# Kernel optimization log

Hardware: AMD Instinct MI355X
Metric: run time of the kernel (lower is better)

Reference implementation:

```python
import jax, jax.numpy as jnp
import numpy as np

N = 50000
E = 800000
F_IN = 128
HEADS = 4
OUT_PER_HEAD = 32  # out_features 128 / 4 heads
NEG_SLOPE = 0.2


def setup_inputs() -> dict:
    key = jax.random.key(0)
    k1, k2, k3, k4, k5 = jax.random.split(key, 5)
    x = jax.random.normal(k1, (N, F_IN), dtype=jnp.float32)
    edge_index = jax.random.randint(k2, (2, E), 0, N, dtype=jnp.int64)
    # xavier-uniform style init
    limW = float(np.sqrt(6.0 / (F_IN + OUT_PER_HEAD)))
    W = jax.random.uniform(k3, (HEADS, F_IN, OUT_PER_HEAD), jnp.float32, -limW, limW)
    lima = float(np.sqrt(6.0 / (OUT_PER_HEAD + 1)))
    a_l = jax.random.uniform(k4, (HEADS, OUT_PER_HEAD), jnp.float32, -lima, lima)
    a_r = jax.random.uniform(k5, (HEADS, OUT_PER_HEAD), jnp.float32, -lima, lima)
    return {"x": x, "edge_index": edge_index, "W": W, "a_l": a_l, "a_r": a_r}


def _leaky_relu(v, slope):
    return jnp.where(v >= 0, v, slope * v)


def reference(x, edge_index, W, a_l, a_r):
    src, dst = edge_index[0], edge_index[1]
    n = x.shape[0]
    # Wh: [heads, N, out_per_head]
    Wh = jnp.einsum('nf,kfh->knh', x, W)
    e_l = jnp.einsum('knh,kh->kn', Wh, a_l)  # [heads, N]
    e_r = jnp.einsum('knh,kh->kn', Wh, a_r)
    # per-edge attention logits [heads, E]
    e = _leaky_relu(e_l[:, src] + e_r[:, dst], NEG_SLOPE)
    # segment softmax over incoming edges of each dst node
    seg_max = jax.vmap(lambda ee: jax.ops.segment_max(ee, dst, num_segments=n))(e)
    seg_max = jnp.maximum(seg_max, -1e9)  # torch init value for empty nodes
    exp_e = jnp.exp(e - seg_max[:, dst])
    denom = jax.vmap(lambda ee: jax.ops.segment_sum(ee, dst, num_segments=n))(exp_e)
    alpha = exp_e / (denom[:, dst] + 1e-16)  # [heads, E]
    # weighted aggregation: [heads, E, out_per_head] scattered into [heads, N, out_per_head]
    weighted = alpha[..., None] * Wh[:, src, :]
    out = jax.vmap(lambda w: jax.ops.segment_sum(w, dst, num_segments=n))(weighted)
    # concat heads -> [N, heads*out_per_head]
    return out.transpose(1, 0, 2).reshape(n, -1)
```

## Files before the change

### kernel.cpp

```cpp
#include <hip/hip_runtime.h>

#define NN 50000
#define NE 800000
#define FIN 128
#define NH 4
#define OPH 32
#define FOUT 128
#define NSLOPE 0.2f
#define NGB ((NN + 63) / 64)
#define BCOLS 144
#define LDA 136
#define BSH 5
#define BUKSZ 32
#define NBUK ((NN + BUKSZ - 1) >> BSH)
#define CHUNK 8192
#define NPB1 ((NE + CHUNK - 1) / CHUNK)
#define SLOTP 32
#define SLOTQ 31
#define SLOTS 64
#define GRID1 (9 * NPB1)

typedef __attribute__((ext_vector_type(8))) short short8v;
typedef __attribute__((ext_vector_type(4))) float f32x4;

static __device__ __forceinline__ unsigned short f2bf(float f) {
  unsigned int u = __float_as_uint(f);
  u += 0x7fffu + ((u >> 16) & 1u);
  return (unsigned short)(u >> 16);
}

__global__ __launch_bounds__(128) void k_prep(
    const float* __restrict__ W, const float* __restrict__ a_l,
    const float* __restrict__ a_r, unsigned short* __restrict__ Bt) {
  const int c = blockIdx.x;
  const int f = threadIdx.x;
  unsigned short v = 0;
  if (c < 128) {
    const int h = c >> 5, o = c & 31;
    v = f2bf(W[h * (FIN * OPH) + f * OPH + o]);
  } else if (c < 136) {
    const int j = c - 128;
    const int h = j & 3;
    const float* __restrict__ av = (j < 4) ? a_l : a_r;
    float s = 0.f;
    for (int o = 0; o < 32; ++o)
      s += W[h * (FIN * OPH) + f * OPH + o] * av[h * OPH + o];
    v = f2bf(s);
  }
  Bt[c * FIN + f] = v;
}

__global__ __launch_bounds__(256) void k_gemm_part(
    const float* __restrict__ x, const unsigned short* __restrict__ Bt,
    const int* __restrict__ src, const int* __restrict__ dst,
    unsigned int* __restrict__ ebuf,
    unsigned short* __restrict__ WhU, float* __restrict__ e_l4,
    float* __restrict__ e_r4) {
  __shared__ union U {
    unsigned short As[64 * LDA];
    int cntl[NBUK];
  } sh;
  const int t = threadIdx.x;
  const int bid = blockIdx.x;

  if ((bid % 9) == 8) {
    const int part = bid / 9;
    const int base = part * CHUNK;
    for (int b = t; b < NBUK; b += 256) sh.cntl[b] = 0;
    __syncthreads();
    unsigned int* __restrict__ myreg = ebuf + (size_t)part * NBUK * SLOTP;
#pragma unroll
    for (int k = 0; k < CHUNK / 256; ++k) {
      const int i = base + k * 256 + t;
      if (i < NE) {
        const int d = dst[i];
        const unsigned int s = (unsigned int)src[i];
        const int b = d >> BSH;
        const int lp = atomicAdd(&sh.cntl[b], 1);
        if (lp < SLOTQ)
          myreg[b * SLOTP + 1 + lp] =
              ((unsigned int)(d & (BUKSZ - 1)) << 16) | s;
      }
    }
    __syncthreads();
    for (int b = t; b < NBUK; b += 256)
      myreg[b * SLOTP] = (unsigned int)min(sh.cntl[b], SLOTQ);
    return;
  }

  const int g = bid - (bid + 1) / 9;
  if (g >= NGB) return;
  const int m0 = g * 64;

#pragma unroll
  for (int i = 0; i < 8; ++i) {
    const int fidx = t + i * 256;
    const int node = fidx >> 5;
    const int fg = fidx & 31;
    const int n = m0 + node;
    float4 v = make_float4(0.f, 0.f, 0.f, 0.f);
    if (n < NN) v = *(const float4*)(x + (size_t)n * FIN + fg * 4);
    ushort4 pk;
    pk.x = f2bf(v.x); pk.y = f2bf(v.y); pk.z = f2bf(v.z); pk.w = f2bf(v.w);
    *(ushort4*)&sh.As[node * LDA + fg * 4] = pk;
  }
  __syncthreads();

  const int w = t >> 6;
  const int l = t & 63;
  const int lr = l & 15;
  const int lk = l >> 4;

  short8v a_frag[4];
#pragma unroll
  for (int kk = 0; kk < 4; ++kk)
    a_frag[kk] = *(const short8v*)&sh.As[(w * 16 + lr) * LDA + kk * 32 + lk * 8];

  f32x4 acc[9];
#pragma unroll
  for (int ct = 0; ct < 9; ++ct) acc[ct] = (f32x4){0.f, 0.f, 0.f, 0.f};

#pragma unroll
  for (int ct = 0; ct < 9; ++ct) {
    const unsigned short* __restrict__ Bp =
        Bt + (ct * 16 + lr) * FIN + lk * 8;
    short8v b0 = *(const short8v*)(Bp);
    short8v b1 = *(const short8v*)(Bp + 32);
    short8v b2 = *(const short8v*)(Bp + 64);
    short8v b3 = *(const short8v*)(Bp + 96);
    acc[ct] = __builtin_amdgcn_mfma_f32_16x16x32_bf16(a_frag[0], b0, acc[ct], 0, 0, 0);
    acc[ct] = __builtin_amdgcn_mfma_f32_16x16x32_bf16(a_frag[1], b1, acc[ct], 0, 0, 0);
    acc[ct] = __builtin_amdgcn_mfma_f32_16x16x32_bf16(a_frag[2], b2, acc[ct], 0, 0, 0);
    acc[ct] = __builtin_amdgcn_mfma_f32_16x16x32_bf16(a_frag[3], b3, acc[ct], 0, 0, 0);
  }

#pragma unroll
  for (int ct = 0; ct < 9; ++ct) {
#pragma unroll
    for (int reg = 0; reg < 4; ++reg) {
      const int n = m0 + w * 16 + lk * 4 + reg;
      if (n >= NN) continue;
      const float v = acc[ct][reg];
      if (ct < 8) {
        WhU[(size_t)n * FOUT + ct * 16 + lr] = f2bf(v);
      } else if (lr < 4) {
        e_l4[n * NH + lr] = v;
      } else if (lr < 8) {
        e_r4[n * NH + (lr - 4)] = v;
      }
    }
  }
}

__global__ __launch_bounds__(256) void k_lists_agg(
    const unsigned int* __restrict__ ebuf,
    const float* __restrict__ e_l4, const float* __restrict__ e_r4,
    const unsigned int* __restrict__ Whh, float* __restrict__ out) {
  __shared__ int lists[BUKSZ][SLOTS];
  __shared__ int cur[BUKSZ];
  __shared__ int pfx[128];
  __shared__ float exs[4][64][4];

  const int b = blockIdx.x;
  const int t = threadIdx.x;
  const int w = t >> 6;
  const int lane = t & 63;

  if (t < BUKSZ) cur[t] = 0;
  if (t < 128)
    pfx[t] = (t < NPB1)
                 ? (int)ebuf[((size_t)t * NBUK + b) * SLOTP]
                 : 0;
  __syncthreads();

  for (int d = 1; d < 128; d <<= 1) {
    int add = 0;
    if (t < 128 && t >= d) add = pfx[t - d];
    __syncthreads();
    if (t < 128) pfx[t] += add;
    __syncthreads();
  }
  const int T = pfx[127];

  for (int tid = t; tid < T; tid += 256) {
    int lo = 0, hi = 127;
    while (lo < hi) {
      const int mid = (lo + hi) >> 1;
      if (pfx[mid] > tid) hi = mid; else lo = mid + 1;
    }
    const int j = lo;
    const int p = tid - (j ? pfx[j - 1] : 0);
    const unsigned int v = ebuf[((size_t)j * NBUK + b) * SLOTP + 1 + p];
    const int idx = (int)(v >> 16);
    const int lp = atomicAdd(&cur[idx], 1);
    if (lp < SLOTS) lists[idx][lp] = (int)(v & 0xFFFFu);
  }
  __syncthreads();

  const int h = lane >> 4;
#pragma unroll
  for (int nl = 0; nl < 8; ++nl) {
    const int idx = w * 8 + nl;
    const int n = (b << BSH) + idx;
    if (n >= NN) continue;
    const int deg = min(cur[idx], SLOTS);
    const float4 ern = *(const float4*)&e_r4[n * NH];

    float e0 = 0.f, e1 = 0.f, e2 = 0.f, e3 = 0.f;
    if (lane < deg) {
      const int s = lists[idx][lane];
      const float4 el = *(const float4*)&e_l4[s * NH];
      float l0 = el.x + ern.x; l0 = (l0 >= 0.f) ? l0 : NSLOPE * l0;
      float l1 = el.y + ern.y; l1 = (l1 >= 0.f) ? l1 : NSLOPE * l1;
      float l2 = el.z + ern.z; l2 = (l2 >= 0.f) ? l2 : NSLOPE * l2;
      float l3 = el.w + ern.w; l3 = (l3 >= 0.f) ? l3 : NSLOPE * l3;
      e0 = __expf(l0); e1 = __expf(l1);
      e2 = __expf(l2); e3 = __expf(l3);
    }
    *(float4*)exs[w][lane] = make_float4(e0, e1, e2, e3);
    float D0 = e0, D1 = e1, D2 = e2, D3 = e3;
#pragma unroll
    for (int mm = 32; mm >= 1; mm >>= 1) {
      D0 += __shfl_xor(D0, mm);
      D1 += __shfl_xor(D1, mm);
      D2 += __shfl_xor(D2, mm);
      D3 += __shfl_xor(D3, mm);
    }

    float acc0 = 0.f, acc1 = 0.f;
    int jl = 0;
    for (; jl + 7 < deg; jl += 8) {
      int sj[8];
#pragma unroll
      for (int u = 0; u < 8; ++u) sj[u] = lists[idx][jl + u];
      unsigned int vv[8];
#pragma unroll
      for (int u = 0; u < 8; ++u) vv[u] = Whh[(size_t)sj[u] * 64 + lane];
#pragma unroll
      for (int u = 0; u < 8; ++u) {
        const float wH = exs[w][jl + u][h];
        acc0 = fmaf(wH, __uint_as_float(vv[u] << 16), acc0);
        acc1 = fmaf(wH, __uint_as_float(vv[u] & 0xffff0000u), acc1);
      }
    }
    for (; jl < deg; ++jl) {
      const int sj = lists[idx][jl];
      const float wH = exs[w][jl][h];
      const unsigned int v = Whh[(size_t)sj * 64 + lane];
      acc0 = fmaf(wH, __uint_as_float(v << 16), acc0);
      acc1 = fmaf(wH, __uint_as_float(v & 0xffff0000u), acc1);
    }

    const float dH = (h == 0) ? D0 : (h == 1) ? D1 : (h == 2) ? D2 : D3;
    const float inv = 1.f / (dH + 1e-16f);
    *(float2*)&out[(size_t)n * FOUT + 2 * lane] =
        make_float2(acc0 * inv, acc1 * inv);
  }
}

extern "C" void kernel_launch(void* const* d_in, const int* in_sizes, int n_in,
                              void* d_out, int out_size, void* d_ws, size_t ws_size,
                              hipStream_t stream) {
  const float* x   = (const float*)d_in[0];
  const int*   ei  = (const int*)d_in[1];
  const float* W   = (const float*)d_in[2];
  const float* a_l = (const float*)d_in[3];
  const float* a_r = (const float*)d_in[4];
  float* out = (float*)d_out;

  const int* src = ei;
  const int* dst = ei + NE;

  unsigned int* Whh = (unsigned int*)d_ws;
  float* e_l4     = (float*)(Whh + (size_t)NN * 64);
  float* e_r4     = e_l4 + NN * NH;
  unsigned short* Bt = (unsigned short*)(e_r4 + NN * NH);
  unsigned int* ebuf = (unsigned int*)(Bt + BCOLS * FIN);
  (void)ws_size; (void)in_sizes; (void)n_in; (void)out_size;

  k_prep<<<BCOLS, 128, 0, stream>>>(W, a_l, a_r, Bt);

  k_gemm_part<<<GRID1, 256, 0, stream>>>(
      x, Bt, src, dst, ebuf, (unsigned short*)Whh, e_l4, e_r4);

  k_lists_agg<<<NBUK, 256, 0, stream>>>(ebuf, e_l4, e_r4, Whh, out);
}
```

Measured before the change: 87.28 us.

## Split partitioning into own kernel with LDS counting sort and coalesced bucket writes

The edge-partitioning blocks move out of the fused GEMM kernel into a separate kernel. It counting-sorts each chunk's edges by destination bucket in shared memory, then writes every 32-slot bucket with one contiguous warp-wide store instead of scattered per-edge writes. This aims to cut uncoalesced global writes, but it adds a kernel launch, a second pass over dst, a serial scan in LDS, and it gives up the overlap between partitioning and the GEMM.

After: 125.7 us. 1.44x slower.

```diff
diff --git a/kernel.cpp b/kernel.cpp
--- a/kernel.cpp
+++ b/kernel.cpp
@@ -18,7 +18,6 @@
 #define SLOTP 32
 #define SLOTQ 31
 #define SLOTS 64
-#define GRID1 (9 * NPB1)
 
 typedef __attribute__((ext_vector_type(8))) short short8v;
 typedef __attribute__((ext_vector_type(4))) float f32x4;
@@ -50,47 +49,82 @@
   Bt[c * FIN + f] = v;
 }
 
-__global__ __launch_bounds__(256) void k_gemm_part(
+__global__ __launch_bounds__(256) void k_part(
+    const int* __restrict__ src, const int* __restrict__ dst,
+    unsigned int* __restrict__ ebuf) {
+  __shared__ int startA[NBUK];
+  __shared__ int wsum[256];
+  __shared__ unsigned int sorted[CHUNK];
+  const int part = blockIdx.x;
+  const int base = part * CHUNK;
+  const int t = threadIdx.x;
+
+  for (int b = t; b < NBUK; b += 256) startA[b] = 0;
+  __syncthreads();
+
+#pragma unroll
+  for (int k = 0; k < CHUNK / 256; ++k) {
+    const int i = base + k * 256 + t;
+    if (i < NE) atomicAdd(&startA[dst[i] >> BSH], 1);
+  }
+  __syncthreads();
+
+  const int L = (NBUK + 255) / 256;
+  const int lo = t * L, hiB = min(lo + L, NBUK);
+  int s = 0;
+  for (int j = lo; j < hiB; ++j) s += startA[j];
+  wsum[t] = s;
+  __syncthreads();
+  for (int d = 1; d < 256; d <<= 1) {
+    const int add = (t >= d) ? wsum[t - d] : 0;
+    __syncthreads();
+    wsum[t] += add;
+    __syncthreads();
+  }
+  int run = t ? wsum[t - 1] : 0;
+  for (int j = lo; j < hiB; ++j) {
+    const int c = startA[j];
+    startA[j] = run;
+    run += c;
+  }
+  __syncthreads();
+
+#pragma unroll
+  for (int k = 0; k < CHUNK / 256; ++k) {
+    const int i = base + k * 256 + t;
+    if (i < NE) {
+      const int d = dst[i];
+      const int b = d >> BSH;
+      const int lp = atomicAdd(&startA[b], 1);
+      sorted[lp] = ((unsigned int)(d & (BUKSZ - 1)) << 16) | (unsigned int)src[i];
+    }
+  }
+  __syncthreads();
+
+  unsigned int* __restrict__ myreg = ebuf + (size_t)part * NBUK * SLOTP;
+  const int g = t >> 5;
+  const int w = t & 31;
+  for (int b0 = 0; b0 < NBUK; b0 += 8) {
+    const int b = b0 + g;
+    if (b < NBUK) {
+      const int e = startA[b];
+      const int s0 = b ? startA[b - 1] : 0;
+      const int c = min(e - s0, SLOTQ);
+      unsigned int val = 0;
+      if (w == 0) val = (unsigned int)c;
+      else if (w - 1 < c) val = sorted[s0 + w - 1];
+      myreg[b * SLOTP + w] = val;
+    }
+  }
+}
+
+__global__ __launch_bounds__(256) void k_gemm(
     const float* __restrict__ x, const unsigned short* __restrict__ Bt,
-    const int* __restrict__ src, const int* __restrict__ dst,
-    unsigned int* __restrict__ ebuf,
     unsigned short* __restrict__ WhU, float* __restrict__ e_l4,
     float* __restrict__ e_r4) {
-  __shared__ union U {
-    unsigned short As[64 * LDA];
-    int cntl[NBUK];
-  } sh;
+  __shared__ unsigned short As[64 * LDA];
   const int t = threadIdx.x;
-  const int bid = blockIdx.x;
-
-  if ((bid % 9) == 8) {
-    const int part = bid / 9;
-    const int base = part * CHUNK;
-    for (int b = t; b < NBUK; b += 256) sh.cntl[b] = 0;
-    __syncthreads();
-    unsigned int* __restrict__ myreg = ebuf + (size_t)part * NBUK * SLOTP;
-#pragma unroll
-    for (int k = 0; k < CHUNK / 256; ++k) {
-      const int i = base + k * 256 + t;
-      if (i < NE) {
-        const int d = dst[i];
-        const unsigned int s = (unsigned int)src[i];
-        const int b = d >> BSH;
-        const int lp = atomicAdd(&sh.cntl[b], 1);
-        if (lp < SLOTQ)
-          myreg[b * SLOTP + 1 + lp] =
-              ((unsigned int)(d & (BUKSZ - 1)) << 16) | s;
-      }
-    }
-    __syncthreads();
-    for (int b = t; b < NBUK; b += 256)
-      myreg[b * SLOTP] = (unsigned int)min(sh.cntl[b], SLOTQ);
-    return;
-  }
-
-  const int g = bid - (bid + 1) / 9;
-  if (g >= NGB) return;
-  const int m0 = g * 64;
+  const int m0 = blockIdx.x * 64;
 
 #pragma unroll
   for (int i = 0; i < 8; ++i) {
@@ -102,7 +136,7 @@
     if (n < NN) v = *(const float4*)(x + (size_t)n * FIN + fg * 4);
     ushort4 pk;
     pk.x = f2bf(v.x); pk.y = f2bf(v.y); pk.z = f2bf(v.z); pk.w = f2bf(v.w);
-    *(ushort4*)&sh.As[node * LDA + fg * 4] = pk;
+    *(ushort4*)&As[node * LDA + fg * 4] = pk;
   }
   __syncthreads();
 
@@ -114,7 +148,7 @@
   short8v a_frag[4];
 #pragma unroll
   for (int kk = 0; kk < 4; ++kk)
-    a_frag[kk] = *(const short8v*)&sh.As[(w * 16 + lr) * LDA + kk * 32 + lk * 8];
+    a_frag[kk] = *(const short8v*)&As[(w * 16 + lr) * LDA + kk * 32 + lk * 8];
 
   f32x4 acc[9];
 #pragma unroll
@@ -280,8 +314,9 @@
 
   k_prep<<<BCOLS, 128, 0, stream>>>(W, a_l, a_r, Bt);
 
-  k_gemm_part<<<GRID1, 256, 0, stream>>>(
-      x, Bt, src, dst, ebuf, (unsigned short*)Whh, e_l4, e_r4);
+  k_part<<<NPB1, 256, 0, stream>>>(src, dst, ebuf);
+
+  k_gemm<<<NGB, 256, 0, stream>>>(x, Bt, (unsigned short*)Whh, e_l4, e_r4);
 
   k_lists_agg<<<NBUK, 256, 0, stream>>>(ebuf, e_l4, e_r4, Whh, out);
 }
```
